# Kernel optimization log

Hardware: AMD Instinct MI355X
Metric: run time of the kernel (lower is better)

Reference implementation:

```python
import jax, jax.numpy as jnp
import numpy as np

B, S, D, H = 16, 512, 1024, 16
DK = D // H
DFF = 4 * D
EPS = 1e-5
NEG = -1e9


def fake_quant(w):
    # EMA int8 symmetric per-tensor fake quantization of weights (inference view)
    scale = jnp.max(jnp.abs(w)) / 127.0
    wq = jnp.round(w / scale) * scale
    # straight-through estimator form (no-op in fwd)
    return w + jax.lax.stop_gradient(wq - w)


def layer_norm(x, g, b):
    mu = jnp.mean(x, axis=-1, keepdims=True)
    var = jnp.mean(jnp.square(x - mu), axis=-1, keepdims=True)
    return (x - mu) * jax.lax.rsqrt(var + EPS) * g + b


def setup_inputs() -> dict:
    key = jax.random.key(0)
    ks = jax.random.split(key, 16)
    std = 0.02
    inp = {
        'x': jax.random.normal(ks[0], (B, S, D), jnp.float32),
        'mask': jax.random.randint(ks[1], (B, 1, S, S), 0, 2, jnp.int32),
        'wq': jax.random.normal(ks[2], (D, D), jnp.float32) * std,
        'bq': jnp.zeros((D,), jnp.float32),
        'wk': jax.random.normal(ks[3], (D, D), jnp.float32) * std,
        'bk': jnp.zeros((D,), jnp.float32),
        'wv': jax.random.normal(ks[4], (D, D), jnp.float32) * std,
        'bv': jnp.zeros((D,), jnp.float32),
        'wo': jax.random.normal(ks[5], (D, D), jnp.float32) * std,
        'bo': jnp.zeros((D,), jnp.float32),
        'w1': jax.random.normal(ks[6], (D, DFF), jnp.float32) * std,
        'b1': jnp.zeros((DFF,), jnp.float32),
        'w2': jax.random.normal(ks[7], (DFF, D), jnp.float32) * std,
        'b2': jnp.zeros((D,), jnp.float32),
        'ln1_g': jnp.ones((D,), jnp.float32),
        'ln1_b': jnp.zeros((D,), jnp.float32),
        'ln2_g': jnp.ones((D,), jnp.float32),
        'ln2_b': jnp.zeros((D,), jnp.float32),
        'layer': 0,
    }
    return inp


def reference(x, mask, wq, bq, wk, bk, wv, bv, wo, bo, w1, b1, w2, b2,
              ln1_g, ln1_b, ln2_g, ln2_b, layer):
    # --- input sublayer: x + attention(LN(x)) (dropout = identity at eval) ---
    h = layer_norm(x, ln1_g, ln1_b)
    q = (h @ fake_quant(wq) + bq).reshape(B, S, H, DK).transpose(0, 2, 1, 3)
    k = (h @ fake_quant(wk) + bk).reshape(B, S, H, DK).transpose(0, 2, 1, 3)
    v = (h @ fake_quant(wv) + bv).reshape(B, S, H, DK).transpose(0, 2, 1, 3)
    scores = jnp.einsum('bhqd,bhkd->bhqk', q, k) * (1.0 / np.sqrt(DK))
    scores = jnp.where(mask == 0, NEG, scores)
    p = jax.nn.softmax(scores, axis=-1)
    attn = jnp.einsum('bhqk,bhkd->bhqd', p, v)
    attn = attn.transpose(0, 2, 1, 3).reshape(B, S, D)
    x = x + (attn @ wo + bo)
    # --- output sublayer: x + FFN(LN(x)), gelu (exact), middle_drop=False ---
    h2 = layer_norm(x, ln2_g, ln2_b)
    ff = jax.nn.gelu(h2 @ w1 + b1, approximate=False) @ w2 + b2
    return x + ff
```

## Files before the change

### kernel.cpp

```cpp
#include <hip/hip_runtime.h>
#include <hip/hip_bf16.h>
#include <math.h>

#define B_   16
#define S_   512
#define D_   1024
#define H_   16
#define DK_  64
#define DFF_ 4096
#define NROW (B_ * S_)
#define NEG_ (-1.0e9f)
#define SCQ_ 0.18033688011112042f

typedef __attribute__((ext_vector_type(8))) short short8v;
typedef __attribute__((ext_vector_type(4))) float f32x4;

__device__ __forceinline__ void load_lds16(const void* g, void* l) {
    __builtin_amdgcn_global_load_lds(
        reinterpret_cast<const __attribute__((address_space(1))) unsigned int*>(
            reinterpret_cast<uintptr_t>(g)),
        reinterpret_cast<__attribute__((address_space(3))) unsigned int*>(
            reinterpret_cast<uintptr_t>(l)),
        16, 0, 0);
}

__device__ __forceinline__ ushort f2bf_raw(float f) {
    __hip_bfloat16 h = __float2bfloat16(f);
    return *(ushort*)&h;
}

__global__ void zero_scales_k(unsigned int* p) {
    if (threadIdx.x < 3) p[threadIdx.x] = 0u;
}

__global__ void maxabs_k(const float* __restrict__ w, unsigned int* __restrict__ out, int n) {
    float m = 0.f;
    for (int i = blockIdx.x * blockDim.x + threadIdx.x; i < n; i += gridDim.x * blockDim.x)
        m = fmaxf(m, fabsf(w[i]));
#pragma unroll
    for (int off = 1; off < 64; off <<= 1)
        m = fmaxf(m, __shfl_xor(m, off));
    __shared__ float red[4];
    const int wave = threadIdx.x >> 6;
    if ((threadIdx.x & 63) == 0) red[wave] = m;
    __syncthreads();
    if (threadIdx.x == 0) {
        m = fmaxf(fmaxf(red[0], red[1]), fmaxf(red[2], red[3]));
        atomicMax(out, __float_as_uint(m));
    }
}

__global__ __launch_bounds__(256) void maskpack_k(
    const int* __restrict__ mask, unsigned long long* __restrict__ bits) {
    const int g = blockIdx.x * 4 + (threadIdx.x >> 6);
    const unsigned long long bm = __ballot(mask[(size_t)g * 64 + (threadIdx.x & 63)] != 0);
    if ((threadIdx.x & 63) == 0) bits[g] = bm;
}

__global__ __launch_bounds__(256) void transq_k(
    const float* __restrict__ W, const unsigned int* __restrict__ smax,
    __hip_bfloat16* __restrict__ Wt, int K, int N)
{
    __shared__ float t[32][33];
    const int n0 = blockIdx.x * 32, k0 = blockIdx.y * 32;
    const int tx = threadIdx.x, ty = threadIdx.y;
    float scale = 1.0f;
    if (smax) scale = __uint_as_float(*smax) * (1.0f / 127.0f);
#pragma unroll
    for (int i = 0; i < 4; ++i) {
        float v = W[(size_t)(k0 + ty + 8 * i) * N + n0 + tx];
        if (smax) v = rintf(v / scale) * scale;
        t[ty + 8 * i][tx] = v;
    }
    __syncthreads();
#pragma unroll
    for (int i = 0; i < 4; ++i)
        Wt[(size_t)(n0 + ty + 8 * i) * K + k0 + tx] = __float2bfloat16(t[tx][ty + 8 * i]);
}

__global__ __launch_bounds__(256) void ln_bf16_k(
    const float* __restrict__ x, const float* __restrict__ g,
    const float* __restrict__ b, __hip_bfloat16* __restrict__ y)
{
    const int row = blockIdx.x;
    const int tid = threadIdx.x;
    const float4 v = *(const float4*)&x[(size_t)row * D_ + tid * 4];

    float s = v.x + v.y + v.z + v.w;
#pragma unroll
    for (int off = 1; off < 64; off <<= 1) s += __shfl_xor(s, off);
    __shared__ float red[8];
    const int wave = tid >> 6, lane = tid & 63;
    if (lane == 0) red[wave] = s;
    __syncthreads();
    s = red[0] + red[1] + red[2] + red[3];
    const float mu = s * (1.0f / (float)D_);

    const float d0 = v.x - mu, d1 = v.y - mu, d2 = v.z - mu, d3 = v.w - mu;
    float sq = d0 * d0 + d1 * d1 + d2 * d2 + d3 * d3;
#pragma unroll
    for (int off = 1; off < 64; off <<= 1) sq += __shfl_xor(sq, off);
    if (lane == 0) red[4 + wave] = sq;
    __syncthreads();
    sq = red[4] + red[5] + red[6] + red[7];
    const float rs = 1.0f / sqrtf(sq * (1.0f / (float)D_) + 1e-5f);

    const float4 gv = *(const float4*)&g[tid * 4];
    const float4 bv = *(const float4*)&b[tid * 4];
    union { ushort4 u4; ushort u[4]; } cv;
    cv.u[0] = f2bf_raw(d0 * rs * gv.x + bv.x);
    cv.u[1] = f2bf_raw(d1 * rs * gv.y + bv.y);
    cv.u[2] = f2bf_raw(d2 * rs * gv.z + bv.z);
    cv.u[3] = f2bf_raw(d3 * rs * gv.w + bv.w);
    *(ushort4*)&y[(size_t)row * D_ + tid * 4] = cv.u4;
}

__device__ __forceinline__ float gelu_f(float v) {
    return 0.5f * v * (1.0f + erff(v * 0.70710678118654752f));
}

template <int EPI, bool OBF>
__global__ __launch_bounds__(256) void gemm_bf16(
    const __hip_bfloat16* __restrict__ A, const __hip_bfloat16* __restrict__ Bt,
    const float* __restrict__ bias, const float* __restrict__ res,
    void* __restrict__ C, int M, int N, int K)
{
    __shared__ __align__(16) __hip_bfloat16 Asm[128 * 64];
    __shared__ __align__(16) __hip_bfloat16 Bsm[128 * 64];

    const int tid = threadIdx.x;
    const int w = tid >> 6, l = tid & 63;
    const int lhi = l >> 4, llo = l & 15;
    const int row0 = blockIdx.y * 128, col0 = blockIdx.x * 128;
    const int wr = w >> 1, wc = w & 1;

    f32x4 acc[4][4] = {};

    const __hip_bfloat16* Ap[4];
    const __hip_bfloat16* Bp[4];
#pragma unroll
    for (int p = 0; p < 4; ++p) {
        const int c = p * 256 + tid;
        const int rr = c >> 3, kseg = c & 7;
        Ap[p] = A + (size_t)(row0 + rr) * K + kseg * 8;
        Bp[p] = Bt + (size_t)(col0 + rr) * K + kseg * 8;
    }
    char* const AsmB = (char*)Asm;
    char* const BsmB = (char*)Bsm;

    for (int k0 = 0; k0 < K; k0 += 64) {
#pragma unroll
        for (int p = 0; p < 4; ++p) {
            load_lds16(Ap[p] + k0, AsmB + p * 4096 + w * 1024);
            load_lds16(Bp[p] + k0, BsmB + p * 4096 + w * 1024);
        }
        __syncthreads();
#pragma unroll
        for (int kk = 0; kk < 2; ++kk) {
            short8v a[4], b[4];
#pragma unroll
            for (int m = 0; m < 4; ++m)
                a[m] = *(const short8v*)&Asm[(wr * 64 + m * 16 + llo) * 64 + kk * 32 + lhi * 8];
#pragma unroll
            for (int n = 0; n < 4; ++n)
                b[n] = *(const short8v*)&Bsm[(wc * 64 + n * 16 + llo) * 64 + kk * 32 + lhi * 8];
#pragma unroll
            for (int m = 0; m < 4; ++m)
#pragma unroll
                for (int n = 0; n < 4; ++n)
                    acc[m][n] = __builtin_amdgcn_mfma_f32_16x16x32_bf16(a[m], b[n], acc[m][n], 0, 0, 0);
        }
        __syncthreads();
    }

#pragma unroll
    for (int n = 0; n < 4; ++n) {
        const int col = col0 + wc * 64 + n * 16 + llo;
        const float bs = bias[col];
#pragma unroll
        for (int m = 0; m < 4; ++m) {
            const int rbase = row0 + wr * 64 + m * 16 + lhi * 4;
#pragma unroll
            for (int j = 0; j < 4; ++j) {
                float v = acc[m][n][j] + bs;
                if (EPI == 1) v = gelu_f(v);
                if (EPI == 2) v += res[(size_t)(rbase + j) * N + col];
                if (OBF) ((__hip_bfloat16*)C)[(size_t)(rbase + j) * N + col] = __float2bfloat16(v);
                else     ((float*)C)[(size_t)(rbase + j) * N + col] = v;
            }
        }
    }
}

__global__ __launch_bounds__(256) void gemm_qkv(
    const __hip_bfloat16* __restrict__ A, const __hip_bfloat16* __restrict__ Wcat,
    const float* __restrict__ bq, const float* __restrict__ bk, const float* __restrict__ bv,
    __hip_bfloat16* __restrict__ qbh, __hip_bfloat16* __restrict__ kbh,
    __hip_bfloat16* __restrict__ vth)
{
    const int K = D_;
    __shared__ __align__(16) __hip_bfloat16 Asm[128 * 64];
    __shared__ __align__(16) __hip_bfloat16 Bsm[128 * 64];

    const int tid = threadIdx.x;
    const int w = tid >> 6, l = tid & 63;
    const int lhi = l >> 4, llo = l & 15;
    const int row0 = blockIdx.y * 128, col0 = blockIdx.x * 128;
    const int wr = w >> 1, wc = w & 1;

    f32x4 acc[4][4] = {};

    const __hip_bfloat16* Ap[4];
    const __hip_bfloat16* Bp[4];
#pragma unroll
    for (int p = 0; p < 4; ++p) {
        const int c = p * 256 + tid;
        const int rr = c >> 3, kseg = c & 7;
        Ap[p] = A + (size_t)(row0 + rr) * K + kseg * 8;
        Bp[p] = Wcat + (size_t)(col0 + rr) * K + kseg * 8;
    }
    char* const AsmB = (char*)Asm;
    char* const BsmB = (char*)Bsm;

    for (int k0 = 0; k0 < K; k0 += 64) {
#pragma unroll
        for (int p = 0; p < 4; ++p) {
            load_lds16(Ap[p] + k0, AsmB + p * 4096 + w * 1024);
            load_lds16(Bp[p] + k0, BsmB + p * 4096 + w * 1024);
        }
        __syncthreads();
#pragma unroll
        for (int kk = 0; kk < 2; ++kk) {
            short8v a[4], b[4];
#pragma unroll
            for (int m = 0; m < 4; ++m)
                a[m] = *(const short8v*)&Asm[(wr * 64 + m * 16 + llo) * 64 + kk * 32 + lhi * 8];
#pragma unroll
            for (int n = 0; n < 4; ++n)
                b[n] = *(const short8v*)&Bsm[(wc * 64 + n * 16 + llo) * 64 + kk * 32 + lhi * 8];
#pragma unroll
            for (int m = 0; m < 4; ++m)
#pragma unroll
                for (int n = 0; n < 4; ++n)
                    acc[m][n] = __builtin_amdgcn_mfma_f32_16x16x32_bf16(a[m], b[n], acc[m][n], 0, 0, 0);
        }
        __syncthreads();
    }

#pragma unroll
    for (int n = 0; n < 4; ++n) {
        const int gcol = col0 + wc * 64 + n * 16 + llo;
        const int proj = gcol >> 10, lcol = gcol & 1023;
        const float bs = (proj == 0 ? bq : (proj == 1 ? bk : bv))[lcol];
#pragma unroll
        for (int m = 0; m < 4; ++m) {
            const int rbase = row0 + wr * 64 + m * 16 + lhi * 4;
            if (proj == 2) {
                const int bb = rbase >> 9, s = rbase & 511;
                const int hh = lcol >> 6, dk = lcol & 63;
                union { ushort4 u4; ushort u[4]; } pk;
#pragma unroll
                for (int j = 0; j < 4; ++j) pk.u[j] = f2bf_raw(acc[m][n][j] + bs);
                *(ushort4*)&((ushort*)vth)[(((size_t)(bb * 16 + hh) * 64 + dk) << 9) + s] = pk.u4;
            } else {
                __hip_bfloat16* dst = proj == 0 ? qbh : kbh;
                const float sc = proj == 0 ? SCQ_ : 1.0f;
#pragma unroll
                for (int j = 0; j < 4; ++j)
                    dst[(size_t)(rbase + j) * D_ + lcol] = __float2bfloat16((acc[m][n][j] + bs) * sc);
            }
        }
    }
}

__global__ __launch_bounds__(256) void attn_mfma_k(
    const __hip_bfloat16* __restrict__ q, const __hip_bfloat16* __restrict__ k,
    const __hip_bfloat16* __restrict__ vt, const unsigned long long* __restrict__ mbits,
    __hip_bfloat16* __restrict__ o)
{
    const int qt = blockIdx.x;
    const int bh = blockIdx.y;
    const int b = bh >> 4, h = bh & 15;

    __shared__ __align__(16) __hip_bfloat16 Qs[64 * 72];
    __shared__ __align__(16) __hip_bfloat16 Ks[64 * 72];
    __shared__ __align__(16) __hip_bfloat16 Vts[64 * 72];
    __shared__ __align__(16) __hip_bfloat16 Pt[64 * 72];

    const int tid = threadIdx.x;
    const int w = tid >> 6, l = tid & 63;
    const int llo = l & 15, lhi = l >> 4;
    const int srow = tid >> 2, schk = tid & 3;

    {
        const __hip_bfloat16* qg =
            q + (size_t)(b * S_ + qt * 64 + srow) * D_ + h * 64 + schk * 16;
        *(short8v*)&Qs[srow * 72 + schk * 16] = *(const short8v*)qg;
        *(short8v*)&Qs[srow * 72 + schk * 16 + 8] = *(const short8v*)(qg + 8);
    }

    const __hip_bfloat16* kptr = k + (size_t)(b * S_ + srow) * D_ + h * 64 + schk * 16;
    const __hip_bfloat16* vptr = vt + (((size_t)(b * 16 + h) * 64 + srow) << 9) + schk * 16;
    short8v kr0 = *(const short8v*)kptr;
    short8v kr1 = *(const short8v*)(kptr + 8);
    short8v vr0 = *(const short8v*)vptr;
    short8v vr1 = *(const short8v*)(vptr + 8);

    __syncthreads();

    const short8v qa0 = *(const short8v*)&Qs[(w * 16 + llo) * 72 + lhi * 8];
    const short8v qa1 = *(const short8v*)&Qs[(w * 16 + llo) * 72 + 32 + lhi * 8];

    const unsigned long long* mrow =
        mbits + (((size_t)(b * S_ + qt * 64 + w * 16 + lhi * 4)) << 3);

    f32x4 oacc[4] = {};
    float m_r[4] = {-INFINITY, -INFINITY, -INFINITY, -INFINITY};
    float l_r[4] = {0.f, 0.f, 0.f, 0.f};

    for (int kt = 0; kt < 8; ++kt) {
        *(short8v*)&Ks[srow * 72 + schk * 16] = kr0;
        *(short8v*)&Ks[srow * 72 + schk * 16 + 8] = kr1;
        *(short8v*)&Vts[srow * 72 + schk * 16] = vr0;
        *(short8v*)&Vts[srow * 72 + schk * 16 + 8] = vr1;
        __syncthreads();

        short8v nk0, nk1, nv0, nv1;
        if (kt < 7) {
            const __hip_bfloat16* kp = kptr + (size_t)(kt + 1) * (64 * D_);
            const __hip_bfloat16* vp = vptr + (kt + 1) * 64;
            nk0 = *(const short8v*)kp;
            nk1 = *(const short8v*)(kp + 8);
            nv0 = *(const short8v*)vp;
            nv1 = *(const short8v*)(vp + 8);
        }

        f32x4 sacc[4] = {};
#pragma unroll
        for (int n = 0; n < 4; ++n)
            sacc[n] = __builtin_amdgcn_mfma_f32_16x16x32_bf16(
                qa0, *(const short8v*)&Ks[(n * 16 + llo) * 72 + lhi * 8], sacc[n], 0, 0, 0);
#pragma unroll
        for (int n = 0; n < 4; ++n)
            sacc[n] = __builtin_amdgcn_mfma_f32_16x16x32_bf16(
                qa1, *(const short8v*)&Ks[(n * 16 + llo) * 72 + 32 + lhi * 8], sacc[n], 0, 0, 0);

#pragma unroll
        for (int j = 0; j < 4; ++j) {
            const unsigned long long mb = mrow[j * 8 + kt];
            const float s0 = ((mb >> llo) & 1ull)        ? sacc[0][j] : NEG_;
            const float s1 = ((mb >> (llo + 16)) & 1ull) ? sacc[1][j] : NEG_;
            const float s2 = ((mb >> (llo + 32)) & 1ull) ? sacc[2][j] : NEG_;
            const float s3 = ((mb >> (llo + 48)) & 1ull) ? sacc[3][j] : NEG_;
            float pm = fmaxf(fmaxf(s0, s1), fmaxf(s2, s3));
            pm = fmaxf(pm, __shfl_xor(pm, 1));
            pm = fmaxf(pm, __shfl_xor(pm, 2));
            pm = fmaxf(pm, __shfl_xor(pm, 4));
            pm = fmaxf(pm, __shfl_xor(pm, 8));
            const float mnew = fmaxf(m_r[j], pm);
            const float alpha = exp2f(m_r[j] - mnew);
            const float p0 = exp2f(s0 - mnew);
            const float p1 = exp2f(s1 - mnew);
            const float p2 = exp2f(s2 - mnew);
            const float p3 = exp2f(s3 - mnew);
            float rsum = p0 + p1 + p2 + p3;
            rsum += __shfl_xor(rsum, 1);
            rsum += __shfl_xor(rsum, 2);
            rsum += __shfl_xor(rsum, 4);
            rsum += __shfl_xor(rsum, 8);
            l_r[j] = l_r[j] * alpha + rsum;
            m_r[j] = mnew;
#pragma unroll
            for (int df = 0; df < 4; ++df) oacc[df][j] *= alpha;
            const int prow = (w * 16 + lhi * 4 + j) * 72;
            Pt[prow + llo]      = __float2bfloat16(p0);
            Pt[prow + llo + 16] = __float2bfloat16(p1);
            Pt[prow + llo + 32] = __float2bfloat16(p2);
            Pt[prow + llo + 48] = __float2bfloat16(p3);
        }

#pragma unroll
        for (int ks = 0; ks < 2; ++ks) {
            const short8v pa = *(const short8v*)&Pt[(w * 16 + llo) * 72 + ks * 32 + lhi * 8];
#pragma unroll
            for (int df = 0; df < 4; ++df) {
                const short8v vb = *(const short8v*)&Vts[(df * 16 + llo) * 72 + ks * 32 + lhi * 8];
                oacc[df] = __builtin_amdgcn_mfma_f32_16x16x32_bf16(pa, vb, oacc[df], 0, 0, 0);
            }
        }
        __syncthreads();

        if (kt < 7) { kr0 = nk0; kr1 = nk1; vr0 = nv0; vr1 = nv1; }
    }

#pragma unroll
    for (int j = 0; j < 4; ++j) {
        const float inv = 1.0f / l_r[j];
        __hip_bfloat16* orow =
            o + (size_t)(b * S_ + qt * 64 + w * 16 + lhi * 4 + j) * D_ + h * 64;
#pragma unroll
        for (int df = 0; df < 4; ++df)
            orow[df * 16 + llo] = __float2bfloat16(oacc[df][j] * inv);
    }
}

extern "C" void kernel_launch(void* const* d_in, const int* in_sizes, int n_in,
                              void* d_out, int out_size, void* d_ws, size_t ws_size,
                              hipStream_t stream)
{
    const float* x    = (const float*)d_in[0];
    const int*   mask = (const int*)d_in[1];
    const float* wq   = (const float*)d_in[2];
    const float* bq   = (const float*)d_in[3];
    const float* wk   = (const float*)d_in[4];
    const float* bk   = (const float*)d_in[5];
    const float* wv   = (const float*)d_in[6];
    const float* bv   = (const float*)d_in[7];
    const float* wo   = (const float*)d_in[8];
    const float* bo   = (const float*)d_in[9];
    const float* w1   = (const float*)d_in[10];
    const float* b1   = (const float*)d_in[11];
    const float* w2   = (const float*)d_in[12];
    const float* b2   = (const float*)d_in[13];
    const float* ln1g = (const float*)d_in[14];
    const float* ln1b = (const float*)d_in[15];
    const float* ln2g = (const float*)d_in[16];
    const float* ln2b = (const float*)d_in[17];
    float* out = (float*)d_out;
    char* ws = (char*)d_ws;

    const size_t MB = 1024 * 1024;
    __hip_bfloat16* hb    = (__hip_bfloat16*)(ws);
    __hip_bfloat16* qbh   = (__hip_bfloat16*)(ws + 16 * MB);
    __hip_bfloat16* kbh   = (__hip_bfloat16*)(ws + 32 * MB);
    __hip_bfloat16* vth   = (__hip_bfloat16*)(ws + 48 * MB);
    __hip_bfloat16* attnb = (__hip_bfloat16*)(ws + 64 * MB);
    __hip_bfloat16* ff1b  = (__hip_bfloat16*)(ws + 16 * MB);
    __hip_bfloat16* wcat  = (__hip_bfloat16*)(ws + 80 * MB);
    __hip_bfloat16* fqqt  = (__hip_bfloat16*)(ws + 80 * MB);
    __hip_bfloat16* fqkt  = (__hip_bfloat16*)(ws + 82 * MB);
    __hip_bfloat16* fqvt  = (__hip_bfloat16*)(ws + 84 * MB);
    __hip_bfloat16* wot   = (__hip_bfloat16*)(ws + 86 * MB);
    __hip_bfloat16* w1t   = (__hip_bfloat16*)(ws + 88 * MB);
    __hip_bfloat16* w2t   = (__hip_bfloat16*)(ws + 96 * MB);
    unsigned int*   scales = (unsigned int*)(ws + 104 * MB);
    unsigned long long* mbits = (unsigned long long*)(ws + 105 * MB);

    const int NW = D_ * D_;

    zero_scales_k<<<1, 64, 0, stream>>>(scales);
    maxabs_k<<<256, 256, 0, stream>>>(wq, scales + 0, NW);
    maxabs_k<<<256, 256, 0, stream>>>(wk, scales + 1, NW);
    maxabs_k<<<256, 256, 0, stream>>>(wv, scales + 2, NW);
    maskpack_k<<<(B_ * S_ * (S_ / 64)) / 4, 256, 0, stream>>>(mask, mbits);

    const dim3 tb(32, 8);
    transq_k<<<dim3(D_ / 32, D_ / 32), tb, 0, stream>>>(wq, scales + 0, fqqt, D_, D_);
    transq_k<<<dim3(D_ / 32, D_ / 32), tb, 0, stream>>>(wk, scales + 1, fqkt, D_, D_);
    transq_k<<<dim3(D_ / 32, D_ / 32), tb, 0, stream>>>(wv, scales + 2, fqvt, D_, D_);
    transq_k<<<dim3(D_ / 32, D_ / 32), tb, 0, stream>>>(wo, nullptr, wot, D_, D_);
    transq_k<<<dim3(DFF_ / 32, D_ / 32), tb, 0, stream>>>(w1, nullptr, w1t, D_, DFF_);
    transq_k<<<dim3(D_ / 32, DFF_ / 32), tb, 0, stream>>>(w2, nullptr, w2t, DFF_, D_);

    ln_bf16_k<<<NROW, 256, 0, stream>>>(x, ln1g, ln1b, hb);

    gemm_qkv<<<dim3(3 * D_ / 128, NROW / 128), 256, 0, stream>>>(
        hb, wcat, bq, bk, bv, qbh, kbh, vth);

    attn_mfma_k<<<dim3(S_ / 64, B_ * H_), 256, 0, stream>>>(qbh, kbh, vth, mbits, attnb);

    const dim3 gD(D_ / 128, NROW / 128);
    gemm_bf16<2, false><<<gD, 256, 0, stream>>>(attnb, wot, bo, x, out, NROW, D_, D_);

    ln_bf16_k<<<NROW, 256, 0, stream>>>(out, ln2g, ln2b, hb);

    gemm_bf16<1, true><<<dim3(DFF_ / 128, NROW / 128), 256, 0, stream>>>(
        hb, w1t, b1, nullptr, ff1b, NROW, DFF_, D_);

    gemm_bf16<2, false><<<gD, 256, 0, stream>>>(ff1b, w2t, b2, out, out, NROW, D_, DFF_);
}
```

Before: 499.9 us.

## Replace GEMMs with double-buffered 256-row tile kernel with swizzled LDS and phased prefetch

Replaces the 128x128 single-buffered GEMM and QKV kernels with one templated 512-thread kernel. It uses 256xBN tiles, double-buffered LDS, an XOR-swizzled LDS layout to avoid bank conflicts, and prefetch of the next K tile spread across four compute phases with manual waitcnt and barriers. It also adds a block-index swizzle for L2 locality and setprio around the MFMA bursts. The aim is to hide global-load latency and raise MFMA utilisation. In exchange, register pressure rises (8xBNT accumulators per thread), and the hand-placed vmcnt waits must match the exact number of loads in flight.

```diff
diff --git a/kernel.cpp b/kernel.cpp
--- a/kernel.cpp
+++ b/kernel.cpp
@@ -29,6 +29,10 @@
     return *(ushort*)&h;
 }
 
+__device__ __forceinline__ float gelu_f(float v) {
+    return 0.5f * v * (1.0f + erff(v * 0.70710678118654752f));
+}
+
 __global__ void zero_scales_k(unsigned int* p) {
     if (threadIdx.x < 3) p[threadIdx.x] = 0u;
 }
@@ -115,159 +119,163 @@
     *(ushort4*)&y[(size_t)row * D_ + tid * 4] = cv.u4;
 }
 
-__device__ __forceinline__ float gelu_f(float v) {
-    return 0.5f * v * (1.0f + erff(v * 0.70710678118654752f));
-}
-
-template <int EPI, bool OBF>
-__global__ __launch_bounds__(256) void gemm_bf16(
+template <int BNT, int EPI>
+__global__ __launch_bounds__(512, 2) void gemm256(
     const __hip_bfloat16* __restrict__ A, const __hip_bfloat16* __restrict__ Bt,
-    const float* __restrict__ bias, const float* __restrict__ res,
-    void* __restrict__ C, int M, int N, int K)
+    const float* __restrict__ bias, const float* __restrict__ bias2,
+    const float* __restrict__ bias3, const float* __restrict__ res,
+    void* __restrict__ C, void* __restrict__ C2, void* __restrict__ C3,
+    int M, int N, int K)
 {
-    __shared__ __align__(16) __hip_bfloat16 Asm[128 * 64];
-    __shared__ __align__(16) __hip_bfloat16 Bsm[128 * 64];
+    constexpr int BN   = BNT * 64;
+    constexpr int ABYT = 256 * 128;
+    constexpr int BBYT = BN * 128;
+    constexpr int BUF  = ABYT + BBYT;
+    constexpr int SB   = BNT / 2;
+    __shared__ __align__(16) char smem[2 * BUF];
 
     const int tid = threadIdx.x;
-    const int w = tid >> 6, l = tid & 63;
-    const int lhi = l >> 4, llo = l & 15;
-    const int row0 = blockIdx.y * 128, col0 = blockIdx.x * 128;
-    const int wr = w >> 1, wc = w & 1;
-
-    f32x4 acc[4][4] = {};
-
-    const __hip_bfloat16* Ap[4];
-    const __hip_bfloat16* Bp[4];
-#pragma unroll
-    for (int p = 0; p < 4; ++p) {
-        const int c = p * 256 + tid;
-        const int rr = c >> 3, kseg = c & 7;
-        Ap[p] = A + (size_t)(row0 + rr) * K + kseg * 8;
-        Bp[p] = Bt + (size_t)(col0 + rr) * K + kseg * 8;
-    }
-    char* const AsmB = (char*)Asm;
-    char* const BsmB = (char*)Bsm;
-
-    for (int k0 = 0; k0 < K; k0 += 64) {
-#pragma unroll
-        for (int p = 0; p < 4; ++p) {
-            load_lds16(Ap[p] + k0, AsmB + p * 4096 + w * 1024);
-            load_lds16(Bp[p] + k0, BsmB + p * 4096 + w * 1024);
+    const int w = tid >> 6, lane = tid & 63;
+    const int llo = lane & 15, lhi = lane >> 4;
+    const int wr = w >> 2, wc = w & 3;
+
+    const int nwg = gridDim.x;
+    const int bid = blockIdx.x;
+    const int swz = (bid & 7) * (nwg >> 3) + (bid >> 3);
+    const int nby = M >> 8;
+    const int by = swz % nby, bx = swz / nby;
+    const int row0 = by * 256, col0 = bx * BN;
+
+    const int cko0 = ((lhi) ^ (llo & 7)) * 16;
+    const int cko1 = ((4 + lhi) ^ (llo & 7)) * 16;
+
+    const int l3 = lane >> 3;
+    const int klog8 = ((lane & 7) ^ l3) * 8;
+    const int rA_base = ((w >> 1) & 3) * 16 + (w & 1) * 8 + l3;
+    const int rB_ws = w * 8 + l3;
+
+    const __hip_bfloat16* Asrc[2][2];
+#pragma unroll
+    for (int h = 0; h < 2; ++h)
+#pragma unroll
+        for (int s = 0; s < 2; ++s)
+            Asrc[h][s] = A + (size_t)(row0 + s * 128 + h * 64 + rA_base) * K + klog8;
+    const __hip_bfloat16* Bsrc[2][2];
+#pragma unroll
+    for (int h = 0; h < 2; ++h)
+#pragma unroll
+        for (int s = 0; s < 2; ++s)
+            Bsrc[h][s] = Bt + (size_t)(col0 + h * (BN / 2) + (SB == 2 ? s * 64 : 0) + rB_ws) * K + klog8;
+
+#define STAGE_A(bufv, hh, tt) do {                                                            \
+    load_lds16(Asrc[hh][0] + (size_t)(tt) * 64, smem + (bufv) * BUF + (hh) * 16384 + w * 1024);        \
+    load_lds16(Asrc[hh][1] + (size_t)(tt) * 64, smem + (bufv) * BUF + (hh) * 16384 + 8192 + w * 1024); \
+} while (0)
+#define STAGE_B(bufv, hh, tt) do {                                                                     \
+    load_lds16(Bsrc[hh][0] + (size_t)(tt) * 64, smem + (bufv) * BUF + ABYT + (hh) * (BBYT / 2) + w * 1024); \
+    if (SB == 2)                                                                                       \
+        load_lds16(Bsrc[hh][1] + (size_t)(tt) * 64, smem + (bufv) * BUF + ABYT + (hh) * (BBYT / 2) + 8192 + w * 1024); \
+} while (0)
+
+    f32x4 acc[8][BNT] = {};
+    const int NT = K >> 6;
+
+    STAGE_B(0, 0, 0); STAGE_B(0, 1, 0); STAGE_A(0, 0, 0); STAGE_A(0, 1, 0);
+    asm volatile("s_waitcnt vmcnt(2)");
+    __builtin_amdgcn_sched_barrier(0);
+    __builtin_amdgcn_s_barrier();
+    __builtin_amdgcn_sched_barrier(0);
+
+    short8v bfr[BNT][2];
+    for (int t = 0; t < NT; ++t) {
+        const int buf = t & 1;
+        const bool more = (t + 1) < NT;
+        char* const base = smem + buf * BUF;
+#pragma unroll
+        for (int ph = 0; ph < 4; ++ph) {
+            if (ph == 0) {
+#pragma unroll
+                for (int n = 0; n < BNT; ++n) {
+                    const int brow = wc * (BNT * 16) + n * 16 + llo;
+                    bfr[n][0] = *(const short8v*)(base + ABYT + brow * 128 + cko0);
+                    bfr[n][1] = *(const short8v*)(base + ABYT + brow * 128 + cko1);
+                }
+            }
+            const int mf0 = ph * 2, mf1 = ph * 2 + 1;
+            const int slot0 = (mf0 >> 2) * 128 + wr * 64 + (mf0 & 3) * 16 + llo;
+            const int slot1 = (mf1 >> 2) * 128 + wr * 64 + (mf1 & 3) * 16 + llo;
+            const short8v a0k0 = *(const short8v*)(base + slot0 * 128 + cko0);
+            const short8v a0k1 = *(const short8v*)(base + slot0 * 128 + cko1);
+            const short8v a1k0 = *(const short8v*)(base + slot1 * 128 + cko0);
+            const short8v a1k1 = *(const short8v*)(base + slot1 * 128 + cko1);
+            if (more) {
+                if (ph == 0) STAGE_B(buf ^ 1, 0, t + 1);
+                if (ph == 1) STAGE_B(buf ^ 1, 1, t + 1);
+                if (ph == 2) STAGE_A(buf ^ 1, 0, t + 1);
+                if (ph == 3) STAGE_A(buf ^ 1, 1, t + 1);
+            }
+            __builtin_amdgcn_s_barrier();
+            __builtin_amdgcn_sched_barrier(0);
+            __builtin_amdgcn_s_setprio(1);
+#pragma unroll
+            for (int n = 0; n < BNT; ++n) {
+                acc[mf0][n] = __builtin_amdgcn_mfma_f32_16x16x32_bf16(a0k0, bfr[n][0], acc[mf0][n], 0, 0, 0);
+                acc[mf0][n] = __builtin_amdgcn_mfma_f32_16x16x32_bf16(a0k1, bfr[n][1], acc[mf0][n], 0, 0, 0);
+                acc[mf1][n] = __builtin_amdgcn_mfma_f32_16x16x32_bf16(a1k0, bfr[n][0], acc[mf1][n], 0, 0, 0);
+                acc[mf1][n] = __builtin_amdgcn_mfma_f32_16x16x32_bf16(a1k1, bfr[n][1], acc[mf1][n], 0, 0, 0);
+            }
+            __builtin_amdgcn_s_setprio(0);
+            if (ph == 1) {
+                if (more) { asm volatile("s_waitcnt vmcnt(%0)" :: "i"(2 * SB)); }
+                else      { asm volatile("s_waitcnt vmcnt(0)"); }
+            }
+            if (ph == 3) { asm volatile("s_waitcnt vmcnt(2)"); }
+            __builtin_amdgcn_sched_barrier(0);
+            __builtin_amdgcn_s_barrier();
+            __builtin_amdgcn_sched_barrier(0);
         }
-        __syncthreads();
-#pragma unroll
-        for (int kk = 0; kk < 2; ++kk) {
-            short8v a[4], b[4];
-#pragma unroll
-            for (int m = 0; m < 4; ++m)
-                a[m] = *(const short8v*)&Asm[(wr * 64 + m * 16 + llo) * 64 + kk * 32 + lhi * 8];
-#pragma unroll
-            for (int n = 0; n < 4; ++n)
-                b[n] = *(const short8v*)&Bsm[(wc * 64 + n * 16 + llo) * 64 + kk * 32 + lhi * 8];
-#pragma unroll
-            for (int m = 0; m < 4; ++m)
-#pragma unroll
-                for (int n = 0; n < 4; ++n)
-                    acc[m][n] = __builtin_amdgcn_mfma_f32_16x16x32_bf16(a[m], b[n], acc[m][n], 0, 0, 0);
-        }
-        __syncthreads();
-    }
-
-#pragma unroll
-    for (int n = 0; n < 4; ++n) {
-        const int col = col0 + wc * 64 + n * 16 + llo;
-        const float bs = bias[col];
-#pragma unroll
-        for (int m = 0; m < 4; ++m) {
-            const int rbase = row0 + wr * 64 + m * 16 + lhi * 4;
-#pragma unroll
-            for (int j = 0; j < 4; ++j) {
-                float v = acc[m][n][j] + bs;
-                if (EPI == 1) v = gelu_f(v);
-                if (EPI == 2) v += res[(size_t)(rbase + j) * N + col];
-                if (OBF) ((__hip_bfloat16*)C)[(size_t)(rbase + j) * N + col] = __float2bfloat16(v);
-                else     ((float*)C)[(size_t)(rbase + j) * N + col] = v;
-            }
-        }
-    }
-}
-
-__global__ __launch_bounds__(256) void gemm_qkv(
-    const __hip_bfloat16* __restrict__ A, const __hip_bfloat16* __restrict__ Wcat,
-    const float* __restrict__ bq, const float* __restrict__ bk, const float* __restrict__ bv,
-    __hip_bfloat16* __restrict__ qbh, __hip_bfloat16* __restrict__ kbh,
-    __hip_bfloat16* __restrict__ vth)
-{
-    const int K = D_;
-    __shared__ __align__(16) __hip_bfloat16 Asm[128 * 64];
-    __shared__ __align__(16) __hip_bfloat16 Bsm[128 * 64];
-
-    const int tid = threadIdx.x;
-    const int w = tid >> 6, l = tid & 63;
-    const int lhi = l >> 4, llo = l & 15;
-    const int row0 = blockIdx.y * 128, col0 = blockIdx.x * 128;
-    const int wr = w >> 1, wc = w & 1;
-
-    f32x4 acc[4][4] = {};
-
-    const __hip_bfloat16* Ap[4];
-    const __hip_bfloat16* Bp[4];
-#pragma unroll
-    for (int p = 0; p < 4; ++p) {
-        const int c = p * 256 + tid;
-        const int rr = c >> 3, kseg = c & 7;
-        Ap[p] = A + (size_t)(row0 + rr) * K + kseg * 8;
-        Bp[p] = Wcat + (size_t)(col0 + rr) * K + kseg * 8;
-    }
-    char* const AsmB = (char*)Asm;
-    char* const BsmB = (char*)Bsm;
-
-    for (int k0 = 0; k0 < K; k0 += 64) {
-#pragma unroll
-        for (int p = 0; p < 4; ++p) {
-            load_lds16(Ap[p] + k0, AsmB + p * 4096 + w * 1024);
-            load_lds16(Bp[p] + k0, BsmB + p * 4096 + w * 1024);
-        }
-        __syncthreads();
-#pragma unroll
-        for (int kk = 0; kk < 2; ++kk) {
-            short8v a[4], b[4];
-#pragma unroll
-            for (int m = 0; m < 4; ++m)
-                a[m] = *(const short8v*)&Asm[(wr * 64 + m * 16 + llo) * 64 + kk * 32 + lhi * 8];
-#pragma unroll
-            for (int n = 0; n < 4; ++n)
-                b[n] = *(const short8v*)&Bsm[(wc * 64 + n * 16 + llo) * 64 + kk * 32 + lhi * 8];
-#pragma unroll
-            for (int m = 0; m < 4; ++m)
-#pragma unroll
-                for (int n = 0; n < 4; ++n)
-                    acc[m][n] = __builtin_amdgcn_mfma_f32_16x16x32_bf16(a[m], b[n], acc[m][n], 0, 0, 0);
-        }
-        __syncthreads();
-    }
-
-#pragma unroll
-    for (int n = 0; n < 4; ++n) {
-        const int gcol = col0 + wc * 64 + n * 16 + llo;
-        const int proj = gcol >> 10, lcol = gcol & 1023;
-        const float bs = (proj == 0 ? bq : (proj == 1 ? bk : bv))[lcol];
-#pragma unroll
-        for (int m = 0; m < 4; ++m) {
-            const int rbase = row0 + wr * 64 + m * 16 + lhi * 4;
-            if (proj == 2) {
-                const int bb = rbase >> 9, s = rbase & 511;
-                const int hh = lcol >> 6, dk = lcol & 63;
-                union { ushort4 u4; ushort u[4]; } pk;
-#pragma unroll
-                for (int j = 0; j < 4; ++j) pk.u[j] = f2bf_raw(acc[m][n][j] + bs);
-                *(ushort4*)&((ushort*)vth)[(((size_t)(bb * 16 + hh) * 64 + dk) << 9) + s] = pk.u4;
-            } else {
-                __hip_bfloat16* dst = proj == 0 ? qbh : kbh;
-                const float sc = proj == 0 ? SCQ_ : 1.0f;
-#pragma unroll
-                for (int j = 0; j < 4; ++j)
-                    dst[(size_t)(rbase + j) * D_ + lcol] = __float2bfloat16((acc[m][n][j] + bs) * sc);
+    }
+#undef STAGE_A
+#undef STAGE_B
+
+#pragma unroll
+    for (int n = 0; n < BNT; ++n) {
+        const int col = col0 + wc * (BNT * 16) + n * 16 + llo;
+        if (EPI == 3) {
+            const int proj = col0 >> 10;
+            const int lcol = col & 1023;
+            const float bs = (proj == 0 ? bias : proj == 1 ? bias2 : bias3)[lcol];
+#pragma unroll
+            for (int mf = 0; mf < 8; ++mf) {
+                const int rbase = row0 + wr * 128 + mf * 16 + lhi * 4;
+                if (proj == 2) {
+                    const int bb = rbase >> 9, srow = rbase & 511;
+                    const int hh = lcol >> 6, dk = lcol & 63;
+                    union { ushort4 u4; ushort u[4]; } pk;
+#pragma unroll
+                    for (int j = 0; j < 4; ++j) pk.u[j] = f2bf_raw(acc[mf][n][j] + bs);
+                    *(ushort4*)&((ushort*)C3)[(((size_t)(bb * 16 + hh) * 64 + dk) << 9) + srow] = pk.u4;
+                } else {
+                    __hip_bfloat16* dst = proj == 0 ? (__hip_bfloat16*)C : (__hip_bfloat16*)C2;
+                    const float sc = proj == 0 ? SCQ_ : 1.0f;
+#pragma unroll
+                    for (int j = 0; j < 4; ++j)
+                        dst[(size_t)(rbase + j) * D_ + lcol] = __float2bfloat16((acc[mf][n][j] + bs) * sc);
+                }
+            }
+        } else {
+            const float bs = bias[col];
+#pragma unroll
+            for (int mf = 0; mf < 8; ++mf) {
+                const int rbase = row0 + wr * 128 + mf * 16 + lhi * 4;
+#pragma unroll
+                for (int j = 0; j < 4; ++j) {
+                    float v = acc[mf][n][j] + bs;
+                    if (EPI == 1) v = gelu_f(v);
+                    if (EPI == 2) v += res[(size_t)(rbase + j) * N + col];
+                    if (EPI == 1) ((__hip_bfloat16*)C)[(size_t)(rbase + j) * N + col] = __float2bfloat16(v);
+                    else          ((float*)C)[(size_t)(rbase + j) * N + col] = v;
+                }
             }
         }
     }
@@ -464,18 +472,19 @@
 
     ln_bf16_k<<<NROW, 256, 0, stream>>>(x, ln1g, ln1b, hb);
 
-    gemm_qkv<<<dim3(3 * D_ / 128, NROW / 128), 256, 0, stream>>>(
-        hb, wcat, bq, bk, bv, qbh, kbh, vth);
+    gemm256<4, 3><<<(3 * D_ / 256) * (NROW / 256), 512, 0, stream>>>(
+        hb, wcat, bq, bk, bv, nullptr, qbh, kbh, vth, NROW, 3 * D_, D_);
 
     attn_mfma_k<<<dim3(S_ / 64, B_ * H_), 256, 0, stream>>>(qbh, kbh, vth, mbits, attnb);
 
-    const dim3 gD(D_ / 128, NROW / 128);
-    gemm_bf16<2, false><<<gD, 256, 0, stream>>>(attnb, wot, bo, x, out, NROW, D_, D_);
+    gemm256<2, 2><<<(D_ / 128) * (NROW / 256), 512, 0, stream>>>(
+        attnb, wot, bo, nullptr, nullptr, x, out, nullptr, nullptr, NROW, D_, D_);
 
     ln_bf16_k<<<NROW, 256, 0, stream>>>(out, ln2g, ln2b, hb);
 
-    gemm_bf16<1, true><<<dim3(DFF_ / 128, NROW / 128), 256, 0, stream>>>(
-        hb, w1t, b1, nullptr, ff1b, NROW, DFF_, D_);
-
-    gemm_bf16<2, false><<<gD, 256, 0, stream>>>(ff1b, w2t, b2, out, out, NROW, D_, DFF_);
-}
+    gemm256<4, 1><<<(DFF_ / 256) * (NROW / 256), 512, 0, stream>>>(
+        hb, w1t, b1, nullptr, nullptr, nullptr, ff1b, nullptr, nullptr, NROW, DFF_, D_);
+
+    gemm256<2, 2><<<(D_ / 128) * (NROW / 256), 512, 0, stream>>>(
+        ff1b, w2t, b2, nullptr, nullptr, out, out, nullptr, nullptr, NROW, D_, DFF_);
+}
```

Result: faster. 454.3 us (-9.1%).
